# Performance work log

Hardware: AMD Instinct MI355X
Metric: run time of the kernel (lower is better)

## Reference

```python
import jax, jax.numpy as jnp
import numpy as np

DIM = 128
QK_DIM = 64
NUM_HEADS = 4
HEAD_DIM = QK_DIM // NUM_HEADS
SCALE = HEAD_DIM ** -0.5
EPS = 1e-6


def setup_inputs() -> dict:
    key = jax.random.key(0)
    ks = jax.random.split(key, 9)
    B, C, H, W = 8, DIM, 128, 128
    K, T = 256, 64
    x = jax.random.normal(ks[0], (B, C, H, W), dtype=jnp.float32)
    joint_probs = jax.random.uniform(ks[1], (B, K), dtype=jnp.float32)
    sims = jax.random.uniform(ks[2], (B, K, T), dtype=jnp.float32)
    indices = jax.random.randint(ks[3], (B, K, T), 0, H * W)
    gamma = jnp.ones((C,), jnp.float32)
    beta = jnp.zeros((C,), jnp.float32)
    Wq = jax.random.normal(ks[4], (QK_DIM, C), jnp.float32) * (C ** -0.5)
    Wk = jax.random.normal(ks[5], (QK_DIM, C), jnp.float32) * (C ** -0.5)
    Wv = jax.random.normal(ks[6], (DIM, C), jnp.float32) * (C ** -0.5)
    return {"x": x, "joint_probs": joint_probs, "sims": sims,
            "gamma": gamma, "beta": beta, "Wq": Wq, "Wk": Wk, "Wv": Wv,
            "indices": indices}


def reference(x, joint_probs, sims, gamma, beta, Wq, Wk, Wv, indices):
    B, C, H, W = x.shape
    HW = H * W
    Bk, K, T = indices.shape
    xf = x.reshape(B, C, HW)
    # LayerNorm2d over channel dim
    mu = jnp.mean(xf, axis=1, keepdims=True)
    var = jnp.var(xf, axis=1, keepdims=True)
    xn = (xf - mu) * jax.lax.rsqrt(var + EPS)
    xn = gamma[None, :, None] * xn + beta[None, :, None]
    # 1x1 convs == channel matmuls
    q = jnp.einsum('dc,bct->bdt', Wq, xn)  # [B, qk_dim, HW]
    k = jnp.einsum('dc,bct->bdt', Wk, xn)
    v = jnp.einsum('dc,bct->bdt', Wv, xn)  # [B, dim, HW]
    b_idx = jnp.arange(B)[:, None, None]
    def gather_sp(arr):  # arr [B, d, HW] -> [B, K, T, d]
        return arr.transpose(0, 2, 1)[b_idx, indices]
    def to_heads(arr):  # [B,K,T,d] -> [B,K,h,T,hd]
        d = arr.shape[-1]
        return arr.reshape(B, K, T, NUM_HEADS, d // NUM_HEADS).transpose(0, 1, 3, 2, 4)
    Q = to_heads(gather_sp(q))
    Kh = to_heads(gather_sp(k))
    V = to_heads(gather_sp(v))  # [B,K,h,T,dim//h]
    attn = jnp.einsum('bkhtc,bkhsc->bkhts', Q, Kh) * SCALE
    attn = joint_probs[:, :, None, None, None] * attn
    attn = jax.nn.softmax(attn, axis=-1)  # normalize_attention 'map'
    out = jnp.einsum('bkhts,bkhsc->bkhtc', attn, V)  # [B,K,h,T,hd]
    # 'b k h t c -> b (h c) (k t)'
    out = out.transpose(0, 2, 4, 1, 3).reshape(B, C, K * T)
    weight = jnp.broadcast_to(sims.reshape(B, 1, K * T), (B, C, K * T))
    idx_flat = indices.reshape(B, K * T)
    def scatter_one(idx, val):  # idx [KT], val [C, KT] -> [C, HW]
        return jnp.zeros((C, HW), val.dtype).at[:, idx].add(val)
    num = jax.vmap(scatter_one)(idx_flat, weight * out)
    den = jax.vmap(scatter_one)(idx_flat, weight)
    # weighted scatter-mean with v as base value (weight 1)
    res = (v + num) / (1.0 + den)
    return res.reshape(B, C, H, W)
```

## Files before the change

kernel.cpp:

```cpp
#include <hip/hip_runtime.h>
#include <hip/hip_bf16.h>
#include <math.h>

#define NB 8
#define NC 128
#define NHW 16384
#define NK 256
#define NT 64
#define SCALE_F 0.25f
#define LN_EPS 1e-6f

typedef short s16x8 __attribute__((ext_vector_type(8)));
typedef float f32x16 __attribute__((ext_vector_type(16)));

union FragU { unsigned u[4]; s16x8 s; };

static __device__ inline unsigned pack2bf(float a, float b) {
  union { __hip_bfloat162 h; unsigned u; } x;
  x.h = __float22bfloat162_rn(make_float2(a, b));
  return x.u;
}
static __device__ inline float bflo(unsigned u) { return __uint_as_float(u << 16); }
static __device__ inline float bfhi(unsigned u) { return __uint_as_float(u & 0xffff0000u); }

__global__ __launch_bounds__(256) void wb_kernel(const float* __restrict__ Wq,
                                                 const float* __restrict__ Wk,
                                                 const float* __restrict__ Wv,
                                                 ushort* __restrict__ Wb) {
  const int t = threadIdx.x;
  const int d = blockIdx.x * 2 + (t >> 7);
  const int c = t & 127;
  float v;
  if (d < 64)       v = Wq[d * NC + c];
  else if (d < 128) v = Wk[(d - 64) * NC + c];
  else              v = Wv[(d - 128) * NC + c];
  Wb[d * NC + c] = (ushort)(pack2bf(v, 0.f) & 0xffffu);
}

__global__ __launch_bounds__(256) void zero_cnt_kernel(int* __restrict__ cnt) {
  cnt[blockIdx.x * 256 + threadIdx.x] = 0;
}

__global__ __launch_bounds__(256) void count_kernel(const int* __restrict__ indices,
                                                    int* __restrict__ cnt) {
  const int g = blockIdx.x * 256 + threadIdx.x;
  const int b = g >> 14;
  atomicAdd(&cnt[(b << 14) + indices[g]], 1);
}

__global__ __launch_bounds__(256) void scan_kernel(const int* __restrict__ cnt,
                                                   int* __restrict__ offs) {
  const int b = blockIdx.x, t = threadIdx.x;
  const int base = (b << 14) + t * 64;
  int s = 0;
  for (int j = 0; j < 64; ++j) s += cnt[base + j];
  __shared__ int sums[256];
  sums[t] = s;
  __syncthreads();
  for (int off = 1; off < 256; off <<= 1) {
    int v = (t >= off) ? sums[t - off] : 0;
    __syncthreads();
    sums[t] += v;
    __syncthreads();
  }
  int run = (t == 0) ? 0 : sums[t - 1];
  for (int j = 0; j < 64; ++j) {
    offs[base + j] = run;
    run += cnt[base + j];
  }
}

__global__ __launch_bounds__(256) void fill_kernel(const int* __restrict__ indices,
                                                   int* __restrict__ offs,
                                                   int* __restrict__ list) {
  const int g = blockIdx.x * 256 + threadIdx.x;
  const int b = g >> 14;
  const int tok = g & 16383;
  const int pos = indices[g];
  const int slot = atomicAdd(&offs[(b << 14) + pos], 1);
  list[(b << 14) + slot] = tok;
}

__global__ __launch_bounds__(256) void ln_proj_kernel(
    const float* __restrict__ x, const float* __restrict__ gamma,
    const float* __restrict__ beta, const ushort* __restrict__ Wb,
    ushort* __restrict__ qkvb) {
  __shared__ __align__(16) ushort xn[64 * 128];
  __shared__ float stats[2][4][64];
  const int t = threadIdx.x;
  const int b = blockIdx.y;
  const int pos0 = blockIdx.x * 64;
  const int p = t & 63;
  const int q = t >> 6;

  float xr[32];
  {
    const float* xb = x + ((size_t)b * NC + q * 32) * NHW + pos0 + p;
#pragma unroll
    for (int j = 0; j < 32; ++j) xr[j] = xb[(size_t)j * NHW];
  }
  float s = 0.f, ss = 0.f;
#pragma unroll
  for (int j = 0; j < 32; ++j) { s += xr[j]; ss = fmaf(xr[j], xr[j], ss); }
  stats[0][q][p] = s;
  stats[1][q][p] = ss;
  __syncthreads();
  const float S  = stats[0][0][p] + stats[0][1][p] + stats[0][2][p] + stats[0][3][p];
  const float SS = stats[1][0][p] + stats[1][1][p] + stats[1][2][p] + stats[1][3][p];
  const float mu = S * (1.0f / 128.0f);
  const float rstd = rsqrtf(SS * (1.0f / 128.0f) - mu * mu + LN_EPS);

#pragma unroll
  for (int sl = 0; sl < 4; ++sl) {
    uint4 pk;
    unsigned* pw = (unsigned*)&pk;
#pragma unroll
    for (int e = 0; e < 4; ++e) {
      const int j = sl * 8 + e * 2;
      const int c0 = q * 32 + j;
      const float a  = gamma[c0]     * ((xr[j]     - mu) * rstd) + beta[c0];
      const float bb = gamma[c0 + 1] * ((xr[j + 1] - mu) * rstd) + beta[c0 + 1];
      pw[e] = pack2bf(a, bb);
    }
    const int slot = (q * 4 + sl) ^ (p & 15);
    *(uint4*)((char*)xn + p * 256 + slot * 16) = pk;
  }
  __syncthreads();

  const int l = t & 63;
  const int cl = l & 31;
  const int hl = l >> 5;

  s16x8 af[2][8];
#pragma unroll
  for (int dt = 0; dt < 2; ++dt) {
    const int d = 64 * q + 32 * dt + cl;
#pragma unroll
    for (int ks = 0; ks < 8; ++ks)
      af[dt][ks] = *(const s16x8*)(Wb + d * NC + ks * 16 + 8 * hl);
  }

  f32x16 acc[2][2];
#pragma unroll
  for (int dt = 0; dt < 2; ++dt)
#pragma unroll
    for (int pt = 0; pt < 2; ++pt)
#pragma unroll
      for (int i = 0; i < 16; ++i) acc[dt][pt][i] = 0.f;

#pragma unroll
  for (int pt = 0; pt < 2; ++pt) {
    const int row = 32 * pt + cl;
#pragma unroll
    for (int ks = 0; ks < 8; ++ks) {
      const int slot = (2 * ks + hl) ^ (row & 15);
      const s16x8 bf = *(const s16x8*)((const char*)xn + row * 256 + slot * 16);
      acc[0][pt] = __builtin_amdgcn_mfma_f32_32x32x16_bf16(af[0][ks], bf, acc[0][pt], 0, 0, 0);
      acc[1][pt] = __builtin_amdgcn_mfma_f32_32x32x16_bf16(af[1][ks], bf, acc[1][pt], 0, 0, 0);
    }
  }

#pragma unroll
  for (int dt = 0; dt < 2; ++dt)
#pragma unroll
    for (int pt = 0; pt < 2; ++pt) {
      ushort* wr = qkvb + ((size_t)b * NHW + pos0 + 32 * pt + cl) * 256 +
                   64 * q + 32 * dt + 4 * hl;
#pragma unroll
      for (int r4 = 0; r4 < 4; ++r4) {
        uint2 pkw;
        pkw.x = pack2bf(acc[dt][pt][4 * r4 + 0], acc[dt][pt][4 * r4 + 1]);
        pkw.y = pack2bf(acc[dt][pt][4 * r4 + 2], acc[dt][pt][4 * r4 + 3]);
        *(uint2*)(wr + r4 * 8) = pkw;
      }
    }
}

__global__ __launch_bounds__(256) void attn_kernel(
    const ushort* __restrict__ qkvb, const int* __restrict__ indices,
    const float* __restrict__ sims, const float* __restrict__ jp,
    ushort* __restrict__ wout) {
  __shared__ __align__(16) ushort kqv[64 * 256];
  __shared__ int idx_s[NT];
  __shared__ float w_s[NT];
  const int t = threadIdx.x;
  const int k = blockIdx.x;
  const int b = blockIdx.y;
  const size_t bh = (size_t)b << 14;

  if (t < NT) {
    const int g = (b * NK + k) * NT + t;
    idx_s[t] = indices[g];
    w_s[t] = sims[g];
  }
  const float sp = SCALE_F * jp[b * NK + k];
  __syncthreads();

  {
    const int w = t >> 6, l = t & 63;
    const int c4 = l * 4;
    const int slot = c4 >> 3;
    const int lowb = (c4 & 7) * 2;
#pragma unroll
    for (int it = 0; it < 16; ++it) {
      const int tok = w * 16 + it;
      const uint2 v = *(const uint2*)&qkvb[(bh + idx_s[tok]) * 256 + c4];
      *(uint2*)((char*)kqv + tok * 512 + ((slot ^ (tok & 7)) << 4) + lowb) = v;
    }
  }
  __syncthreads();

  const int h = t >> 6;
  const int l = t & 63;
  const int c = l & 31;
  const int hl = l >> 5;

  s16x8 qf[2], kf[2];
  {
    const int slotq = h * 2 + hl;
    const int slotk = 8 + h * 2 + hl;
#pragma unroll
    for (int tt = 0; tt < 2; ++tt) {
      const int row = 32 * tt + c;
      qf[tt] = *(const s16x8*)((const char*)kqv + row * 512 + ((slotq ^ (row & 7)) << 4));
    }
#pragma unroll
    for (int at = 0; at < 2; ++at) {
      const int row = 32 * at + c;
      kf[at] = *(const s16x8*)((const char*)kqv + row * 512 + ((slotk ^ (row & 7)) << 4));
    }
  }

  f32x16 sacc[2][2];
#pragma unroll
  for (int at = 0; at < 2; ++at)
#pragma unroll
    for (int tt = 0; tt < 2; ++tt) {
#pragma unroll
      for (int i = 0; i < 16; ++i) sacc[at][tt][i] = 0.f;
      sacc[at][tt] = __builtin_amdgcn_mfma_f32_32x32x16_bf16(kf[at], qf[tt], sacc[at][tt], 0, 0, 0);
    }

  unsigned pkv[2][2][8];
#pragma unroll
  for (int tt = 0; tt < 2; ++tt) {
    float m = -1e30f;
#pragma unroll
    for (int at = 0; at < 2; ++at)
#pragma unroll
      for (int i = 0; i < 16; ++i) m = fmaxf(m, sacc[at][tt][i]);
    m = fmaxf(m, __shfl_xor(m, 32));
    float sum = 0.f;
#pragma unroll
    for (int at = 0; at < 2; ++at)
#pragma unroll
      for (int i = 0; i < 16; ++i) {
        const float e = __expf((sacc[at][tt][i] - m) * sp);
        sacc[at][tt][i] = e;
        sum += e;
      }
    sum += __shfl_xor(sum, 32);
    const float inv = w_s[32 * tt + c] / sum;
#pragma unroll
    for (int at = 0; at < 2; ++at)
#pragma unroll
      for (int pi = 0; pi < 8; ++pi)
        pkv[at][tt][pi] = pack2bf(sacc[at][tt][2 * pi] * inv, sacc[at][tt][2 * pi + 1] * inv);
  }

  f32x16 oac[2];
#pragma unroll
  for (int tt = 0; tt < 2; ++tt)
#pragma unroll
    for (int i = 0; i < 16; ++i) oac[tt][i] = 0.f;

  const int slotv = 16 + h * 4 + (c >> 3);
  const int lowv = (c & 7) * 2;
#pragma unroll
  for (int ks = 0; ks < 4; ++ks) {
    const int at = ks >> 1;
    const int ksb = 16 * ks + 8 * hl;
    FragU vf;
#pragma unroll
    for (int jj = 0; jj < 4; ++jj) {
      const unsigned lo =
          *(const ushort*)((const char*)kqv + (ksb + 2 * jj) * 512 + ((slotv ^ (2 * jj)) << 4) + lowv);
      const unsigned hi =
          *(const ushort*)((const char*)kqv + (ksb + 2 * jj + 1) * 512 + ((slotv ^ (2 * jj + 1)) << 4) + lowv);
      vf.u[jj] = lo | (hi << 16);
    }
#pragma unroll
    for (int tt = 0; tt < 2; ++tt) {
      const int base = 4 * (ks & 1);
      const unsigned o0 = pkv[at][tt][base + 0];
      const unsigned o1 = pkv[at][tt][base + 1];
      const unsigned o2 = pkv[at][tt][base + 2];
      const unsigned o3 = pkv[at][tt][base + 3];
      const unsigned s0 = hl ? o0 : o2;
      const unsigned s1 = hl ? o1 : o3;
      const unsigned y0 = __shfl_xor(s0, 32);
      const unsigned y1 = __shfl_xor(s1, 32);
      FragU pf;
      pf.u[0] = hl ? y0 : o0;
      pf.u[1] = hl ? y1 : o1;
      pf.u[2] = hl ? o2 : y0;
      pf.u[3] = hl ? o3 : y1;
      oac[tt] = __builtin_amdgcn_mfma_f32_32x32x16_bf16(vf.s, pf.s, oac[tt], 0, 0, 0);
    }
  }

#pragma unroll
  for (int tt = 0; tt < 2; ++tt) {
    ushort* wr = wout + ((bh + (size_t)k * 64 + 32 * tt + c) << 7) + h * 32 + 4 * hl;
#pragma unroll
    for (int pi = 0; pi < 4; ++pi) {
      uint2 pkw;
      pkw.x = pack2bf(oac[tt][4 * pi + 0], oac[tt][4 * pi + 1]);
      pkw.y = pack2bf(oac[tt][4 * pi + 2], oac[tt][4 * pi + 3]);
      *(uint2*)(wr + pi * 8) = pkw;
    }
  }
}

__global__ __launch_bounds__(256) void final_gather(
    const ushort* __restrict__ qkvb, const ushort* __restrict__ wout,
    const float* __restrict__ sims, const int* __restrict__ cnt,
    const int* __restrict__ offs, const int* __restrict__ list,
    float* __restrict__ out) {
  __shared__ __align__(16) float res[64][132];
  __shared__ float invd[64];
  __shared__ int cnt_s[64], st_s[64];
  const int t = threadIdx.x;
  const int pos0 = blockIdx.x * 64;
  const int b = blockIdx.y;
  const size_t bh = (size_t)b << 14;

  if (t < 64) {
    const int p = pos0 + t;
    const int c = cnt[bh + p];
    cnt_s[t] = c;
    st_s[t] = offs[bh + p] - c;
  }
#pragma unroll
  for (int it = 0; it < 8; ++it) {
    const int f = t + it * 256;
    const int row = f >> 5;
    const int c4 = (f & 31) * 4;
    const uint2 v = *(const uint2*)&qkvb[(bh + pos0 + row) * 256 + 128 + c4];
    res[row][c4 + 0] = bflo(v.x);
    res[row][c4 + 1] = bfhi(v.x);
    res[row][c4 + 2] = bflo(v.y);
    res[row][c4 + 3] = bfhi(v.y);
  }
  __syncthreads();

  if (t < 64) {
    float s = 0.f;
    const int n = cnt_s[t], st = st_s[t];
    for (int j = 0; j < n; ++j) {
      const int tok = list[bh + st + j];
      s += sims[bh + tok];
    }
    invd[t] = 1.0f / (1.0f + s);
  }
  __syncthreads();

  {
    const int w = t >> 6, l = t & 63;
    for (int p16 = 0; p16 < 16; ++p16) {
      const int p = w * 16 + p16;
      const int n = cnt_s[p], st = st_s[p];
      if (n) {
        float2 a = *(float2*)&res[p][l * 2];
        for (int j = 0; j < n; ++j) {
          const int tok = list[bh + st + j];
          const unsigned u = ((const unsigned*)(wout + ((bh + tok) << 7)))[l];
          a.x += bflo(u);
          a.y += bfhi(u);
        }
        res[p][l * 2] = a.x;
        res[p][l * 2 + 1] = a.y;
      }
    }
  }
  __syncthreads();

  {
    const int px = t & 63;
    const int cg = t >> 6;
    const float inv = invd[px];
#pragma unroll
    for (int it = 0; it < 32; ++it) {
      const int c = cg * 32 + it;
      out[(bh << 7) + (size_t)c * NHW + pos0 + px] = res[px][c] * inv;
    }
  }
}

extern "C" void kernel_launch(void* const* d_in, const int* in_sizes, int n_in,
                              void* d_out, int out_size, void* d_ws, size_t ws_size,
                              hipStream_t stream) {
  (void)in_sizes; (void)n_in; (void)out_size; (void)ws_size;
  const float* x     = (const float*)d_in[0];
  const float* jp    = (const float*)d_in[1];
  const float* sims  = (const float*)d_in[2];
  const float* gamma = (const float*)d_in[3];
  const float* beta  = (const float*)d_in[4];
  const float* Wq    = (const float*)d_in[5];
  const float* Wk    = (const float*)d_in[6];
  const float* Wv    = (const float*)d_in[7];
  const int* indices = (const int*)d_in[8];
  float* out = (float*)d_out;

  char* ws = (char*)d_ws;
  ushort* qkvb = (ushort*)ws;
  ushort* wout = (ushort*)(ws + 67108864);
  ushort* Wb   = (ushort*)(ws + 100663296);
  int*    cnt  = (int*)(ws + 100728832);
  int*    offs = (int*)(ws + 101253120);
  int*    list = (int*)(ws + 101777408);

  zero_cnt_kernel<<<dim3(512), 256, 0, stream>>>(cnt);
  count_kernel<<<dim3(512), 256, 0, stream>>>(indices, cnt);
  wb_kernel<<<dim3(128), 256, 0, stream>>>(Wq, Wk, Wv, Wb);
  ln_proj_kernel<<<dim3(NHW / 64, NB), 256, 0, stream>>>(x, gamma, beta, Wb, qkvb);
  scan_kernel<<<dim3(NB), 256, 0, stream>>>(cnt, offs);
  fill_kernel<<<dim3(512), 256, 0, stream>>>(indices, offs, list);
  attn_kernel<<<dim3(NK, NB), 256, 0, stream>>>(qkvb, indices, sims, jp, wout);
  final_gather<<<dim3(NHW / 64, NB), 256, 0, stream>>>(qkvb, wout, sims, cnt,
                                                       offs, list, out);
}
```

Before: 254.7 us.

## Vectorize LN loads, stage projection output through LDS, and widen gathers

```diff
diff --git a/kernel.cpp b/kernel.cpp
--- a/kernel.cpp
+++ b/kernel.cpp
@@ -22,6 +22,8 @@
 }
 static __device__ inline float bflo(unsigned u) { return __uint_as_float(u << 16); }
 static __device__ inline float bfhi(unsigned u) { return __uint_as_float(u & 0xffff0000u); }
+
+static __device__ inline int xcd_swz(int bx) { return ((bx & 7) << 5) | (bx >> 3); }
 
 __global__ __launch_bounds__(256) void wb_kernel(const float* __restrict__ Wq,
                                                  const float* __restrict__ Wk,
@@ -85,45 +87,81 @@
     const float* __restrict__ x, const float* __restrict__ gamma,
     const float* __restrict__ beta, const ushort* __restrict__ Wb,
     ushort* __restrict__ qkvb) {
-  __shared__ __align__(16) ushort xn[64 * 128];
-  __shared__ float stats[2][4][64];
+  __shared__ __align__(16) ushort qbuf[64 * 256];
+  __shared__ __align__(16) float stats_s[2][4][64];
   const int t = threadIdx.x;
   const int b = blockIdx.y;
-  const int pos0 = blockIdx.x * 64;
-  const int p = t & 63;
-  const int q = t >> 6;
-
-  float xr[32];
-  {
-    const float* xb = x + ((size_t)b * NC + q * 32) * NHW + pos0 + p;
-#pragma unroll
-    for (int j = 0; j < 32; ++j) xr[j] = xb[(size_t)j * NHW];
-  }
-  float s = 0.f, ss = 0.f;
-#pragma unroll
-  for (int j = 0; j < 32; ++j) { s += xr[j]; ss = fmaf(xr[j], xr[j], ss); }
-  stats[0][q][p] = s;
-  stats[1][q][p] = ss;
-  __syncthreads();
-  const float S  = stats[0][0][p] + stats[0][1][p] + stats[0][2][p] + stats[0][3][p];
-  const float SS = stats[1][0][p] + stats[1][1][p] + stats[1][2][p] + stats[1][3][p];
-  const float mu = S * (1.0f / 128.0f);
-  const float rstd = rsqrtf(SS * (1.0f / 128.0f) - mu * mu + LN_EPS);
-
-#pragma unroll
-  for (int sl = 0; sl < 4; ++sl) {
-    uint4 pk;
-    unsigned* pw = (unsigned*)&pk;
-#pragma unroll
-    for (int e = 0; e < 4; ++e) {
-      const int j = sl * 8 + e * 2;
-      const int c0 = q * 32 + j;
-      const float a  = gamma[c0]     * ((xr[j]     - mu) * rstd) + beta[c0];
-      const float bb = gamma[c0 + 1] * ((xr[j + 1] - mu) * rstd) + beta[c0 + 1];
-      pw[e] = pack2bf(a, bb);
-    }
-    const int slot = (q * 4 + sl) ^ (p & 15);
-    *(uint4*)((char*)xn + p * 256 + slot * 16) = pk;
+  const int pos0 = xcd_swz(blockIdx.x) * 64;
+  const int c16 = t & 15;
+  const int cg = t >> 4;
+
+  float4 xv[8];
+  {
+    const float* xb = x + ((size_t)b * NC + cg * 8) * NHW + pos0 + c16 * 4;
+#pragma unroll
+    for (int j = 0; j < 8; ++j) xv[j] = *(const float4*)(xb + (size_t)j * NHW);
+  }
+
+  float s[4], ss[4];
+#pragma unroll
+  for (int pp = 0; pp < 4; ++pp) { s[pp] = 0.f; ss[pp] = 0.f; }
+#pragma unroll
+  for (int j = 0; j < 8; ++j) {
+    const float* f = (const float*)&xv[j];
+#pragma unroll
+    for (int pp = 0; pp < 4; ++pp) { s[pp] += f[pp]; ss[pp] = fmaf(f[pp], f[pp], ss[pp]); }
+  }
+#pragma unroll
+  for (int pp = 0; pp < 4; ++pp) {
+    s[pp] += __shfl_xor(s[pp], 16);  ss[pp] += __shfl_xor(ss[pp], 16);
+    s[pp] += __shfl_xor(s[pp], 32);  ss[pp] += __shfl_xor(ss[pp], 32);
+  }
+  const int w = t >> 6;
+  if ((cg & 3) == 0) {
+    *(float4*)&stats_s[0][w][c16 * 4] = make_float4(s[0], s[1], s[2], s[3]);
+    *(float4*)&stats_s[1][w][c16 * 4] = make_float4(ss[0], ss[1], ss[2], ss[3]);
+  }
+  __syncthreads();
+  float4 S = *(float4*)&stats_s[0][0][c16 * 4];
+  float4 SS = *(float4*)&stats_s[1][0][c16 * 4];
+#pragma unroll
+  for (int ww = 1; ww < 4; ++ww) {
+    const float4 a = *(float4*)&stats_s[0][ww][c16 * 4];
+    const float4 bb = *(float4*)&stats_s[1][ww][c16 * 4];
+    S.x += a.x; S.y += a.y; S.z += a.z; S.w += a.w;
+    SS.x += bb.x; SS.y += bb.y; SS.z += bb.z; SS.w += bb.w;
+  }
+  float mu[4], rstd[4];
+  {
+    const float* Sp = (const float*)&S;
+    const float* SSp = (const float*)&SS;
+#pragma unroll
+    for (int pp = 0; pp < 4; ++pp) {
+      mu[pp] = Sp[pp] * (1.0f / 128.0f);
+      rstd[pp] = rsqrtf(SSp[pp] * (1.0f / 128.0f) - mu[pp] * mu[pp] + LN_EPS);
+    }
+  }
+
+  {
+    float g[8], be[8];
+#pragma unroll
+    for (int j = 0; j < 8; ++j) { g[j] = gamma[cg * 8 + j]; be[j] = beta[cg * 8 + j]; }
+#pragma unroll
+    for (int pp = 0; pp < 4; ++pp) {
+      const int p_loc = c16 * 4 + pp;
+      uint4 pk;
+      unsigned* pw = (unsigned*)&pk;
+#pragma unroll
+      for (int e = 0; e < 4; ++e) {
+        const float* f0 = (const float*)&xv[2 * e];
+        const float* f1 = (const float*)&xv[2 * e + 1];
+        const float a0 = g[2 * e] * ((f0[pp] - mu[pp]) * rstd[pp]) + be[2 * e];
+        const float a1 = g[2 * e + 1] * ((f1[pp] - mu[pp]) * rstd[pp]) + be[2 * e + 1];
+        pw[e] = pack2bf(a0, a1);
+      }
+      const int slot = cg ^ (p_loc & 15);
+      *(uint4*)((char*)qbuf + p_loc * 256 + slot * 16) = pk;
+    }
   }
   __syncthreads();
 
@@ -134,7 +172,7 @@
   s16x8 af[2][8];
 #pragma unroll
   for (int dt = 0; dt < 2; ++dt) {
-    const int d = 64 * q + 32 * dt + cl;
+    const int d = 64 * w + 32 * dt + cl;
 #pragma unroll
     for (int ks = 0; ks < 8; ++ks)
       af[dt][ks] = *(const s16x8*)(Wb + d * NC + ks * 16 + 8 * hl);
@@ -154,26 +192,39 @@
 #pragma unroll
     for (int ks = 0; ks < 8; ++ks) {
       const int slot = (2 * ks + hl) ^ (row & 15);
-      const s16x8 bf = *(const s16x8*)((const char*)xn + row * 256 + slot * 16);
+      const s16x8 bf = *(const s16x8*)((const char*)qbuf + row * 256 + slot * 16);
       acc[0][pt] = __builtin_amdgcn_mfma_f32_32x32x16_bf16(af[0][ks], bf, acc[0][pt], 0, 0, 0);
       acc[1][pt] = __builtin_amdgcn_mfma_f32_32x32x16_bf16(af[1][ks], bf, acc[1][pt], 0, 0, 0);
     }
   }
+  __syncthreads();
 
 #pragma unroll
   for (int dt = 0; dt < 2; ++dt)
 #pragma unroll
     for (int pt = 0; pt < 2; ++pt) {
-      ushort* wr = qkvb + ((size_t)b * NHW + pos0 + 32 * pt + cl) * 256 +
-                   64 * q + 32 * dt + 4 * hl;
+      const int pos = 32 * pt + cl;
 #pragma unroll
       for (int r4 = 0; r4 < 4; ++r4) {
+        const int slot16 = 8 * w + 4 * dt + r4;
         uint2 pkw;
         pkw.x = pack2bf(acc[dt][pt][4 * r4 + 0], acc[dt][pt][4 * r4 + 1]);
         pkw.y = pack2bf(acc[dt][pt][4 * r4 + 2], acc[dt][pt][4 * r4 + 3]);
-        *(uint2*)(wr + r4 * 8) = pkw;
+        *(uint2*)((char*)qbuf + pos * 512 + ((slot16 ^ (pos & 31)) << 4) + 8 * hl) = pkw;
       }
     }
+  __syncthreads();
+
+  {
+    const size_t base = ((size_t)b * NHW + pos0) * 256;
+#pragma unroll
+    for (int it = 0; it < 16; ++it) {
+      const int r = it * 4 + w;
+      const uint2 v = *(const uint2*)((const char*)qbuf + r * 512 +
+                                      (((l >> 1) ^ (r & 31)) << 4) + (l & 1) * 8);
+      *(uint2*)(qkvb + base + r * 256 + l * 4) = v;
+    }
+  }
 }
 
 __global__ __launch_bounds__(256) void attn_kernel(
@@ -197,15 +248,15 @@
   __syncthreads();
 
   {
-    const int w = t >> 6, l = t & 63;
-    const int c4 = l * 4;
-    const int slot = c4 >> 3;
-    const int lowb = (c4 & 7) * 2;
-#pragma unroll
-    for (int it = 0; it < 16; ++it) {
-      const int tok = w * 16 + it;
-      const uint2 v = *(const uint2*)&qkvb[(bh + idx_s[tok]) * 256 + c4];
-      *(uint2*)((char*)kqv + tok * 512 + ((slot ^ (tok & 7)) << 4) + lowb) = v;
+    const int w = t >> 6;
+    const int l = t & 63;
+    const int half = l >> 5;
+    const int sl = l & 31;
+#pragma unroll
+    for (int it = 0; it < 8; ++it) {
+      const int tok = w * 16 + it * 2 + half;
+      const uint4 v = *(const uint4*)&qkvb[(bh + idx_s[tok]) * 256 + sl * 8];
+      *(uint4*)((char*)kqv + tok * 512 + ((sl ^ (tok & 7)) << 4)) = v;
     }
   }
   __syncthreads();
@@ -331,7 +382,7 @@
   __shared__ float invd[64];
   __shared__ int cnt_s[64], st_s[64];
   const int t = threadIdx.x;
-  const int pos0 = blockIdx.x * 64;
+  const int pos0 = xcd_swz(blockIdx.x) * 64;
   const int b = blockIdx.y;
   const size_t bh = (size_t)b << 14;
 
@@ -342,15 +393,19 @@
     st_s[t] = offs[bh + p] - c;
   }
 #pragma unroll
-  for (int it = 0; it < 8; ++it) {
+  for (int it = 0; it < 4; ++it) {
     const int f = t + it * 256;
-    const int row = f >> 5;
-    const int c4 = (f & 31) * 4;
-    const uint2 v = *(const uint2*)&qkvb[(bh + pos0 + row) * 256 + 128 + c4];
-    res[row][c4 + 0] = bflo(v.x);
-    res[row][c4 + 1] = bfhi(v.x);
-    res[row][c4 + 2] = bflo(v.y);
-    res[row][c4 + 3] = bfhi(v.y);
+    const int row = f >> 4;
+    const int c8 = (f & 15) * 8;
+    const uint4 v = *(const uint4*)&qkvb[(bh + pos0 + row) * 256 + 128 + c8];
+    res[row][c8 + 0] = bflo(v.x);
+    res[row][c8 + 1] = bfhi(v.x);
+    res[row][c8 + 2] = bflo(v.y);
+    res[row][c8 + 3] = bfhi(v.y);
+    res[row][c8 + 4] = bflo(v.z);
+    res[row][c8 + 5] = bfhi(v.z);
+    res[row][c8 + 6] = bflo(v.w);
+    res[row][c8 + 7] = bfhi(v.w);
   }
   __syncthreads();
 
```

Measured after the change: 239.3 us. 1.06x faster.
